# Kernel tuning notes

Measured on AMD Instinct MI355X. Metric: run time of the kernel, lower is better.

The kernel has to match this reference:

```python
import jax, jax.numpy as jnp
import numpy as np


def setup_inputs() -> dict:
    key = jax.random.key(0)
    ks = jax.random.split(key, 10)
    N, S, H = 500000, 128, 64
    s = lambda k, shape, fan_in: jax.random.normal(k, shape, dtype=jnp.float32) / np.sqrt(fan_in)
    return {
        "my_state": jax.random.normal(ks[0], (S,), dtype=jnp.float32),
        "neighbor_states": jax.random.normal(ks[1], (N, S), dtype=jnp.float32),
        "embed_w": s(ks[2], (S, H), S),
        "embed_b": s(ks[3], (H,), S),
        "key_w": s(ks[4], (H, H), H),
        "key_b": s(ks[5], (H,), H),
        "query_w": s(ks[6], (S + H, H), S + H),
        "query_b": s(ks[7], (H,), S + H),
        "attn_w": s(ks[8], (2 * H, 1), 2 * H),
        "attn_b": s(ks[9], (1,), 2 * H),
    }


def reference(my_state, neighbor_states, embed_w, embed_b, key_w, key_b,
              query_w, query_b, attn_w, attn_b):
    H = embed_w.shape[1]
    # per-neighbor embeddings and keys: [N, H]
    emb = neighbor_states @ embed_w + embed_b
    keys = emb @ key_w + key_b
    # query from own state + mean neighbor embedding: [H]
    mean_emb = emb.mean(axis=0)
    query = jnp.concatenate([my_state, mean_emb], axis=-1) @ query_w + query_b
    # attention_net(cat(query, key)) split so we never materialize [N, 2H]
    wq, wk = attn_w[:H, 0], attn_w[H:, 0]
    scores = keys @ wk + (query @ wq + attn_b[0])  # [N]
    attention_weights = jax.nn.softmax(scores, axis=0)  # [N]
    weighted_embedding = attention_weights @ emb  # [H]
    return weighted_embedding, attention_weights
```

## Files before the change

### kernel.cpp

```cpp
#include <hip/hip_runtime.h>
#include <math.h>


#define S_DIM  128
#define H_DIM  64
#define NBLK   2048

typedef float f4 __attribute__((ext_vector_type(4)));

__global__ void k_precompute_u(const float* __restrict__ embed_w,
                               const float* __restrict__ key_w,
                               const float* __restrict__ attn_w,
                               float* __restrict__ u)
{
    __shared__ float kv[H_DIM];
    const int t = threadIdx.x;
    if (t < H_DIM) {
        float acc = 0.f;
        #pragma unroll 8
        for (int j = 0; j < H_DIM; ++j) acc += key_w[t * H_DIM + j] * attn_w[H_DIM + j];
        kv[t] = acc;
    }
    __syncthreads();
    float acc = 0.f;
    #pragma unroll 8
    for (int h = 0; h < H_DIM; ++h) acc += embed_w[t * H_DIM + h] * kv[h];
    u[t] = acc;
}

__global__ __launch_bounds__(256) void k_pass1(
    const float* __restrict__ X,
    const float* __restrict__ u,
    float* __restrict__ scores_out,
    float* __restrict__ pz,
    float* __restrict__ pt_t,
    int N)
{
    const int tid  = threadIdx.x;
    const int lane = tid & 63;
    const int w    = tid >> 6;
    const int l16  = lane & 15;
    const int g    = lane >> 4;

    const f4 uLo = *(const f4*)(u + 4 * l16);
    const f4 uHi = *(const f4*)(u + H_DIM + 4 * l16);

    const int quads = (N + 3) >> 2;
    const int qs = (int)(((long long)blockIdx.x       * quads) / NBLK);
    const int qe = (int)(((long long)(blockIdx.x + 1) * quads) / NBLK);

    auto loadrow = [&](int q, f4& lo, f4& hi) {
        int row = 4 * q + g;
        row = row < N ? row : N - 1;
        const float* p = X + (size_t)row * S_DIM;
        lo = __builtin_nontemporal_load((const f4*)(p + 4 * l16));
        hi = __builtin_nontemporal_load((const f4*)(p + H_DIM + 4 * l16));
    };

    float Z  = 0.f;
    f4 tLo = (f4)(0.f);
    f4 tHi = (f4)(0.f);

    int q = qs + w;
    f4 lo, hi;
    loadrow(q, lo, hi);

    while (q < qe) {
        f4 nlo, nhi;
        loadrow(q + 4, nlo, nhi);

        float s8 = lo.x * uLo.x + lo.y * uLo.y + lo.z * uLo.z + lo.w * uLo.w
                 + hi.x * uHi.x + hi.y * uHi.y + hi.z * uHi.z + hi.w * uHi.w;
        s8 += __shfl_xor(s8, 1);
        s8 += __shfl_xor(s8, 2);
        s8 += __shfl_xor(s8, 4);
        s8 += __shfl_xor(s8, 8);

        const int  row = 4 * q + g;
        const bool v   = row < N;
        if (l16 == 0 && v) scores_out[row] = s8;

        const float e = v ? __expf(s8) : 0.f;
        Z   += e;
        tLo += e * lo;
        tHi += e * hi;

        lo = nlo; hi = nhi; q += 4;
    }

    auto red2 = [](float v) { v += __shfl_xor(v, 16); v += __shfl_xor(v, 32); return v; };
    tLo.x = red2(tLo.x); tLo.y = red2(tLo.y); tLo.z = red2(tLo.z); tLo.w = red2(tLo.w);
    tHi.x = red2(tHi.x); tHi.y = red2(tHi.y); tHi.z = red2(tHi.z); tHi.w = red2(tHi.w);
    Z = red2(Z);

    __shared__ float sT[4][S_DIM];
    __shared__ float sZ[4];
    if (lane < 16) {
        *(f4*)(&sT[w][4 * l16])         = tLo;
        *(f4*)(&sT[w][H_DIM + 4 * l16]) = tHi;
    }
    if (lane == 0) sZ[w] = Z;
    __syncthreads();

    if (tid < S_DIM)
        pt_t[(size_t)tid * NBLK + blockIdx.x] = sT[0][tid] + sT[1][tid] + sT[2][tid] + sT[3][tid];
    else if (tid == S_DIM)
        pz[blockIdx.x] = sZ[0] + sZ[1] + sZ[2] + sZ[3];
}

__global__ __launch_bounds__(256) void k_pass2(
    const float* __restrict__ pz, const float* __restrict__ pt_t,
    float* __restrict__ tS,
    float* __restrict__ zstar)
{
    const int k   = blockIdx.x;
    const int tid = threadIdx.x;
    __shared__ float red[256];

    float z = 0.f;
    for (int b = tid; b < NBLK; b += 256) z += pz[b];
    red[tid] = z; __syncthreads();
    for (int s = 128; s; s >>= 1) { if (tid < s) red[tid] += red[tid + s]; __syncthreads(); }
    const float Z = red[0]; __syncthreads();

    float tacc = 0.f;
    for (int b = tid; b < NBLK; b += 256) tacc += pt_t[(size_t)k * NBLK + b];
    red[tid] = tacc; __syncthreads();
    for (int s = 128; s; s >>= 1) { if (tid < s) red[tid] += red[tid + s]; __syncthreads(); }

    if (tid == 0) {
        tS[k] = red[0] / Z;
        if (k == 0) zstar[0] = Z;
    }
}

__global__ __launch_bounds__(256) void k_pass3(
    float* __restrict__ sw, const float* __restrict__ zstar,
    const float* __restrict__ tS, const float* __restrict__ embed_w,
    const float* __restrict__ embed_b, float* __restrict__ out_emb, int N)
{
    const int tid = threadIdx.x;
    if (blockIdx.x == 0) {
        if (tid < H_DIM) {
            float acc = embed_b[tid];
            #pragma unroll 8
            for (int k = 0; k < S_DIM; ++k) acc += tS[k] * embed_w[k * H_DIM + tid];
            out_emb[tid] = acc;
        } else if (tid == H_DIM) {
            const float invZ = 1.0f / zstar[0];
            for (int i = (N >> 2) << 2; i < N; ++i) sw[i] = __expf(sw[i]) * invZ;
        }
        return;
    }
    const float invZ = 1.0f / zstar[0];
    const int n4 = N >> 2;
    const int stride = (gridDim.x - 1) * 256;
    for (int i = (blockIdx.x - 1) * 256 + tid; i < n4; i += stride) {
        f4 v = ((f4*)sw)[i];
        v.x = __expf(v.x) * invZ;
        v.y = __expf(v.y) * invZ;
        v.z = __expf(v.z) * invZ;
        v.w = __expf(v.w) * invZ;
        ((f4*)sw)[i] = v;
    }
}

extern "C" void kernel_launch(void* const* d_in, const int* in_sizes, int n_in,
                              void* d_out, int out_size, void* d_ws, size_t ws_size,
                              hipStream_t stream) {
    const float* X       = (const float*)d_in[1];
    const float* embed_w = (const float*)d_in[2];
    const float* embed_b = (const float*)d_in[3];
    const float* key_w   = (const float*)d_in[4];
    const float* attn_w  = (const float*)d_in[8];
    float* out = (float*)d_out;

    const int N = in_sizes[1] / S_DIM;

    float* ws    = (float*)d_ws;
    float* zstar = ws;
    float* u     = ws + 64;
    float* tS    = ws + 192;
    float* pz    = ws + 320;
    float* pt_t  = pz + NBLK;

    float* out_emb = out;
    float* out_w   = out + H_DIM;

    k_precompute_u<<<1, 128, 0, stream>>>(embed_w, key_w, attn_w, u);
    k_pass1<<<NBLK, 256, 0, stream>>>(X, u, out_w, pz, pt_t, N);
    k_pass2<<<S_DIM, 256, 0, stream>>>(pz, pt_t, tS, zstar);
    const int nb3 = ((N >> 2) + 255) / 256 + 1;
    k_pass3<<<nb3, 256, 0, stream>>>(out_w, zstar, tS, embed_w, embed_b, out_emb, N);
}
```

Baseline: 66.80 us.

## Fuse all passes into one cooperative kernel with grid sync and LDS-held exponents

Replaces the four-kernel pipeline (precompute u, stream pass, reduction, normalization) with a single cooperative kernel. Each block recomputes u locally, streams its rows, and keeps the per-row exponentials in shared memory. After a grid-wide sync it normalizes those values directly into the output and reduces per-block partials for the weighted embedding. This removes extra launches, the global scratch round trip for scores, and the separate exp/normalize pass. In exchange it uses fewer blocks, sized by occupancy, which could lower memory-level parallelism, and it adds the cost of a grid barrier. The old path is kept as a fallback.

```diff
diff --git a/kernel.cpp b/kernel.cpp
--- a/kernel.cpp
+++ b/kernel.cpp
@@ -1,12 +1,155 @@
 #include <hip/hip_runtime.h>
+#include <hip/hip_cooperative_groups.h>
 #include <math.h>
 
-
-#define S_DIM  128
-#define H_DIM  64
-#define NBLK   2048
+namespace cg = cooperative_groups;
+
+
+#define S_DIM   128
+#define H_DIM   64
+#define MAXROWS 1024
+#define NBLK_FB 2048
 
 typedef float f4 __attribute__((ext_vector_type(4)));
+
+__global__ __launch_bounds__(256, 4) void k_fused(
+    const float* __restrict__ X,
+    const float* __restrict__ embed_w,
+    const float* __restrict__ embed_b,
+    const float* __restrict__ key_w,
+    const float* __restrict__ attn_w,
+    float* __restrict__ out_emb,
+    float* __restrict__ out_w,
+    float* __restrict__ pz,
+    float* __restrict__ pv_t,
+    int N)
+{
+    __shared__ float s_kv[H_DIM];
+    __shared__ float s_u[S_DIM];
+    __shared__ float sT[4][S_DIM];
+    __shared__ float sZ[4];
+    __shared__ float s_e[MAXROWS];
+    __shared__ float red[256];
+
+    const int tid  = threadIdx.x;
+    const int bid  = blockIdx.x;
+    const int nblk = gridDim.x;
+
+    if (tid < H_DIM) {
+        float acc = 0.f;
+        #pragma unroll 8
+        for (int j = 0; j < H_DIM; ++j) acc += key_w[tid * H_DIM + j] * attn_w[H_DIM + j];
+        s_kv[tid] = acc;
+    }
+    __syncthreads();
+    if (tid < S_DIM) {
+        float acc = 0.f;
+        #pragma unroll 8
+        for (int h = 0; h < H_DIM; ++h) acc += embed_w[tid * H_DIM + h] * s_kv[h];
+        s_u[tid] = acc;
+    }
+    __syncthreads();
+
+    const int lane = tid & 63;
+    const int w    = tid >> 6;
+    const int l16  = lane & 15;
+    const int g    = lane >> 4;
+
+    const f4 uLo = *(const f4*)(s_u + 4 * l16);
+    const f4 uHi = *(const f4*)(s_u + H_DIM + 4 * l16);
+
+    const int quads = (N + 3) >> 2;
+    const int qs = (int)(((long long)bid       * quads) / nblk);
+    const int qe = (int)(((long long)(bid + 1) * quads) / nblk);
+
+    auto loadrow = [&](int q, f4& lo, f4& hi) {
+        int row = 4 * q + g;
+        row = row < N ? row : N - 1;
+        const float* p = X + (size_t)row * S_DIM;
+        lo = __builtin_nontemporal_load((const f4*)(p + 4 * l16));
+        hi = __builtin_nontemporal_load((const f4*)(p + H_DIM + 4 * l16));
+    };
+
+    float Z  = 0.f;
+    f4 tLo = (f4)(0.f);
+    f4 tHi = (f4)(0.f);
+
+    int q = qs + w;
+    f4 lo, hi;
+    loadrow(q, lo, hi);
+
+    while (q < qe) {
+        f4 nlo, nhi;
+        loadrow(q + 4, nlo, nhi);
+
+        float s8 = lo.x * uLo.x + lo.y * uLo.y + lo.z * uLo.z + lo.w * uLo.w
+                 + hi.x * uHi.x + hi.y * uHi.y + hi.z * uHi.z + hi.w * uHi.w;
+        s8 += __shfl_xor(s8, 1);
+        s8 += __shfl_xor(s8, 2);
+        s8 += __shfl_xor(s8, 4);
+        s8 += __shfl_xor(s8, 8);
+
+        const int  row = 4 * q + g;
+        const bool v   = row < N;
+        const float e  = v ? __expf(s8) : 0.f;
+        if (l16 == 0 && v) s_e[row - 4 * qs] = e;
+        Z   += e;
+        tLo += e * lo;
+        tHi += e * hi;
+
+        lo = nlo; hi = nhi; q += 4;
+    }
+
+    auto red2 = [](float v) { v += __shfl_xor(v, 16); v += __shfl_xor(v, 32); return v; };
+    tLo.x = red2(tLo.x); tLo.y = red2(tLo.y); tLo.z = red2(tLo.z); tLo.w = red2(tLo.w);
+    tHi.x = red2(tHi.x); tHi.y = red2(tHi.y); tHi.z = red2(tHi.z); tHi.w = red2(tHi.w);
+    Z = red2(Z);
+
+    if (lane < 16) {
+        *(f4*)(&sT[w][4 * l16])         = tLo;
+        *(f4*)(&sT[w][H_DIM + 4 * l16]) = tHi;
+    }
+    if (lane == 0) sZ[w] = Z;
+    __syncthreads();
+
+    if (tid == 0) pz[bid] = sZ[0] + sZ[1] + sZ[2] + sZ[3];
+
+    {
+        const int h = tid & 63, quarter = tid >> 6;
+        float acc = 0.f;
+        #pragma unroll 8
+        for (int k = 32 * quarter; k < 32 * quarter + 32; ++k) {
+            const float tk = sT[0][k] + sT[1][k] + sT[2][k] + sT[3][k];
+            acc += tk * embed_w[k * H_DIM + h];
+        }
+        red[tid] = acc;
+        __syncthreads();
+        if (tid < H_DIM)
+            pv_t[(size_t)tid * nblk + bid] = red[tid] + red[tid + 64] + red[tid + 128] + red[tid + 192];
+    }
+
+    cg::this_grid().sync();
+
+    float z = 0.f;
+    for (int i = tid; i < nblk; i += 256) z += pz[i];
+    red[tid] = z; __syncthreads();
+    for (int s = 128; s; s >>= 1) { if (tid < s) red[tid] += red[tid + s]; __syncthreads(); }
+    const float invZ = 1.0f / red[0];
+    __syncthreads();
+
+    const int r0    = 4 * qs;
+    const int nrows = min(4 * qe, N) - r0;
+    for (int j = tid; j < nrows; j += 256)
+        out_w[r0 + j] = s_e[j] * invZ;
+
+    if (bid < H_DIM) {
+        float a = 0.f;
+        for (int i = tid; i < nblk; i += 256) a += pv_t[(size_t)bid * nblk + i];
+        red[tid] = a; __syncthreads();
+        for (int s = 128; s; s >>= 1) { if (tid < s) red[tid] += red[tid + s]; __syncthreads(); }
+        if (tid == 0) out_emb[bid] = red[0] * invZ + embed_b[bid];
+    }
+}
 
 __global__ void k_precompute_u(const float* __restrict__ embed_w,
                                const float* __restrict__ key_w,
@@ -29,12 +172,9 @@
 }
 
 __global__ __launch_bounds__(256) void k_pass1(
-    const float* __restrict__ X,
-    const float* __restrict__ u,
-    float* __restrict__ scores_out,
-    float* __restrict__ pz,
-    float* __restrict__ pt_t,
-    int N)
+    const float* __restrict__ X, const float* __restrict__ u,
+    float* __restrict__ scores_out, float* __restrict__ pz,
+    float* __restrict__ pt_t, int N)
 {
     const int tid  = threadIdx.x;
     const int lane = tid & 63;
@@ -46,8 +186,8 @@
     const f4 uHi = *(const f4*)(u + H_DIM + 4 * l16);
 
     const int quads = (N + 3) >> 2;
-    const int qs = (int)(((long long)blockIdx.x       * quads) / NBLK);
-    const int qe = (int)(((long long)(blockIdx.x + 1) * quads) / NBLK);
+    const int qs = (int)(((long long)blockIdx.x       * quads) / NBLK_FB);
+    const int qe = (int)(((long long)(blockIdx.x + 1) * quads) / NBLK_FB);
 
     auto loadrow = [&](int q, f4& lo, f4& hi) {
         int row = 4 * q + g;
@@ -57,37 +197,25 @@
         hi = __builtin_nontemporal_load((const f4*)(p + H_DIM + 4 * l16));
     };
 
-    float Z  = 0.f;
-    f4 tLo = (f4)(0.f);
-    f4 tHi = (f4)(0.f);
-
+    float Z = 0.f;
+    f4 tLo = (f4)(0.f), tHi = (f4)(0.f);
     int q = qs + w;
     f4 lo, hi;
     loadrow(q, lo, hi);
-
     while (q < qe) {
         f4 nlo, nhi;
         loadrow(q + 4, nlo, nhi);
-
         float s8 = lo.x * uLo.x + lo.y * uLo.y + lo.z * uLo.z + lo.w * uLo.w
                  + hi.x * uHi.x + hi.y * uHi.y + hi.z * uHi.z + hi.w * uHi.w;
-        s8 += __shfl_xor(s8, 1);
-        s8 += __shfl_xor(s8, 2);
-        s8 += __shfl_xor(s8, 4);
-        s8 += __shfl_xor(s8, 8);
-
+        s8 += __shfl_xor(s8, 1); s8 += __shfl_xor(s8, 2);
+        s8 += __shfl_xor(s8, 4); s8 += __shfl_xor(s8, 8);
         const int  row = 4 * q + g;
         const bool v   = row < N;
         if (l16 == 0 && v) scores_out[row] = s8;
-
         const float e = v ? __expf(s8) : 0.f;
-        Z   += e;
-        tLo += e * lo;
-        tHi += e * hi;
-
+        Z += e; tLo += e * lo; tHi += e * hi;
         lo = nlo; hi = nhi; q += 4;
     }
-
     auto red2 = [](float v) { v += __shfl_xor(v, 16); v += __shfl_xor(v, 32); return v; };
     tLo.x = red2(tLo.x); tLo.y = red2(tLo.y); tLo.z = red2(tLo.z); tLo.w = red2(tLo.w);
     tHi.x = red2(tHi.x); tHi.y = red2(tHi.y); tHi.z = red2(tHi.z); tHi.w = red2(tHi.w);
@@ -103,28 +231,27 @@
     __syncthreads();
 
     if (tid < S_DIM)
-        pt_t[(size_t)tid * NBLK + blockIdx.x] = sT[0][tid] + sT[1][tid] + sT[2][tid] + sT[3][tid];
+        pt_t[(size_t)tid * NBLK_FB + blockIdx.x] = sT[0][tid] + sT[1][tid] + sT[2][tid] + sT[3][tid];
     else if (tid == S_DIM)
         pz[blockIdx.x] = sZ[0] + sZ[1] + sZ[2] + sZ[3];
 }
 
 __global__ __launch_bounds__(256) void k_pass2(
     const float* __restrict__ pz, const float* __restrict__ pt_t,
-    float* __restrict__ tS,
-    float* __restrict__ zstar)
+    float* __restrict__ tS, float* __restrict__ zstar)
 {
     const int k   = blockIdx.x;
     const int tid = threadIdx.x;
     __shared__ float red[256];
 
     float z = 0.f;
-    for (int b = tid; b < NBLK; b += 256) z += pz[b];
+    for (int b = tid; b < NBLK_FB; b += 256) z += pz[b];
     red[tid] = z; __syncthreads();
     for (int s = 128; s; s >>= 1) { if (tid < s) red[tid] += red[tid + s]; __syncthreads(); }
     const float Z = red[0]; __syncthreads();
 
     float tacc = 0.f;
-    for (int b = tid; b < NBLK; b += 256) tacc += pt_t[(size_t)k * NBLK + b];
+    for (int b = tid; b < NBLK_FB; b += 256) tacc += pt_t[(size_t)k * NBLK_FB + b];
     red[tid] = tacc; __syncthreads();
     for (int s = 128; s; s >>= 1) { if (tid < s) red[tid] += red[tid + s]; __syncthreads(); }
 
@@ -175,20 +302,37 @@
     const float* attn_w  = (const float*)d_in[8];
     float* out = (float*)d_out;
 
-    const int N = in_sizes[1] / S_DIM;
+    int N = in_sizes[1] / S_DIM;
+
+    float* out_emb = out;
+    float* out_w   = out + H_DIM;
+
+    int maxb = 0;
+    (void)hipOccupancyMaxActiveBlocksPerMultiprocessor(&maxb, k_fused, 256, 0);
+    int nblk = maxb * 256;
+    if (nblk > 1024) nblk = 1024;
+
+    bool coop_ok = (nblk >= 512);
+    if (coop_ok) {
+        float* pz   = (float*)d_ws;
+        float* pv_t = pz + nblk;
+        void* args[] = { (void*)&X, (void*)&embed_w, (void*)&embed_b, (void*)&key_w,
+                         (void*)&attn_w, (void*)&out_emb, (void*)&out_w,
+                         (void*)&pz, (void*)&pv_t, (void*)&N };
+        hipError_t err = hipLaunchCooperativeKernel((const void*)k_fused, dim3(nblk), dim3(256),
+                                                    args, 0, stream);
+        if (err == hipSuccess) return;
+    }
 
     float* ws    = (float*)d_ws;
     float* zstar = ws;
     float* u     = ws + 64;
     float* tS    = ws + 192;
     float* pz    = ws + 320;
-    float* pt_t  = pz + NBLK;
-
-    float* out_emb = out;
-    float* out_w   = out + H_DIM;
+    float* pt_t  = pz + NBLK_FB;
 
     k_precompute_u<<<1, 128, 0, stream>>>(embed_w, key_w, attn_w, u);
-    k_pass1<<<NBLK, 256, 0, stream>>>(X, u, out_w, pz, pt_t, N);
+    k_pass1<<<NBLK_FB, 256, 0, stream>>>(X, u, out_w, pz, pt_t, N);
     k_pass2<<<S_DIM, 256, 0, stream>>>(pz, pt_t, tS, zstar);
     const int nb3 = ((N >> 2) + 255) / 256 + 1;
     k_pass3<<<nb3, 256, 0, stream>>>(out_w, zstar, tS, embed_w, embed_b, out_emb, N);
```

Result: slower. 151.0 us (+126.1%).
